# Kernel tuning notes

Measured on AMD Instinct MI355X. Metric: run time of the kernel, lower is better.

The kernel has to match this reference:

```python
import jax, jax.numpy as jnp
import numpy as np

TOP_K = 6  # num_experts_per_tok


def _glu_mlp(x, wg, wu, wd):
    # DeepSeek MLP: down( silu(gate(x)) * up(x) )
    return (jax.nn.silu(x @ wg) * (x @ wu)) @ wd


def setup_inputs() -> dict:
    key = jax.random.key(0)
    ks = jax.random.split(key, 8)
    B, S, D, E, F, FS = 2, 2048, 1024, 8, 512, 1024
    sc = 0.02
    return {
        "hidden_states": jax.random.normal(ks[0], (B, S, D), jnp.float32),
        "router_w": jax.random.normal(ks[1], (D, E), jnp.float32) * sc,
        "w_gate": jax.random.normal(ks[2], (E, D, F), jnp.float32) * sc,
        "w_up": jax.random.normal(ks[3], (E, D, F), jnp.float32) * sc,
        "w_down": jax.random.normal(ks[4], (E, F, D), jnp.float32) * sc,
        "ws_gate": jax.random.normal(ks[5], (D, FS), jnp.float32) * sc,
        "ws_up": jax.random.normal(ks[6], (D, FS), jnp.float32) * sc,
        "ws_down": jax.random.normal(ks[7], (FS, D), jnp.float32) * sc,
    }


def reference(hidden_states, router_w, w_gate, w_up, w_down, ws_gate, ws_up, ws_down):
    B, S, D = hidden_states.shape
    x = hidden_states.reshape(-1, D)                       # [T, D] tokens
    # Gate: softmax router + top-k (DeepSeek gate, no renorm)
    scores = jax.nn.softmax(x @ router_w, axis=-1)         # [T, E]
    topk_w, topk_idx = jax.lax.top_k(scores, TOP_K)        # [T, K]
    # Expert SiLU-GLU MLPs evaluated for all experts (math-identical to the
    # argsort dispatch -> grouped GEMM -> scatter combine in moe_infer)
    g = jnp.einsum('td,edf->etf', x, w_gate)               # [E, T, F]
    u = jnp.einsum('td,edf->etf', x, w_up)                 # [E, T, F]
    f_all = jnp.einsum('etf,efd->ted', jax.nn.silu(g) * u, w_down)  # [T, E, D]
    # Combine: final[t] = sum_k topk_w[t,k] * expert_{topk_idx[t,k]}(x[t])
    picked = jnp.take_along_axis(f_all, topk_idx[:, :, None], axis=1)  # [T, K, D]
    y = jnp.sum(picked * topk_w[:, :, None], axis=1).reshape(B, S, D)
    # shared experts branch
    y = y + _glu_mlp(hidden_states, ws_gate, ws_up, ws_down)
    return y
```

## Files before the change

### kernel.cpp

```cpp
#include <hip/hip_runtime.h>

typedef __attribute__((ext_vector_type(8))) short bf16x8;
typedef __attribute__((ext_vector_type(4))) float floatx4;

static __device__ __forceinline__ float b2f(unsigned short u) {
  union { unsigned int i; float f; } v; v.i = ((unsigned int)u) << 16; return v.f;
}
static __device__ __forceinline__ unsigned short f2b(float f) {
  union { float f; unsigned int i; } v; v.f = f;
  unsigned int x = v.i;
  return (unsigned short)((x + 0x7fffu + ((x >> 16) & 1u)) >> 16);
}

#define GLDS(gp, lp) \
  __builtin_amdgcn_global_load_lds( \
      (const __attribute__((address_space(1))) unsigned int*)(gp), \
      (__attribute__((address_space(3))) unsigned int*)(lp), 16, 0, 0)

static __device__ __forceinline__ void swizzle_mn(int lin, int Mb, int Nb,
                                                  int& m_idx, int& n_idx) {
  if ((Mb & 7) == 0) {
    int xcd = lin & 7;
    int idx = lin >> 3;
    int nstrips = Mb >> 3;
    m_idx = (idx % nstrips) * 8 + xcd;
    n_idx = idx / nstrips;
  } else {
    m_idx = lin % Mb;
    n_idx = lin / Mb;
  }
}

__global__ void cvt_f32_bf16(const float* __restrict__ src,
                             unsigned short* __restrict__ dst) {
  int i = (blockIdx.x * 256 + threadIdx.x) * 4;
  float4 v = *(const float4*)(src + i);
  ushort4 o;
  o.x = f2b(v.x); o.y = f2b(v.y); o.z = f2b(v.z); o.w = f2b(v.w);
  *(ushort4*)(dst + i) = o;
}

__global__ void transpose_f32_bf16_2(const float* __restrict__ sA,
                                     unsigned short* __restrict__ dA, int nzA,
                                     const float* __restrict__ sB,
                                     unsigned short* __restrict__ dB,
                                     int K, int N) {
  __shared__ unsigned short tile[32][33];
  int z = blockIdx.z;
  const float* src;
  unsigned short* dst;
  if (z < nzA) { src = sA + (size_t)z * K * N; dst = dA + (size_t)z * K * N; }
  else { src = sB + (size_t)(z - nzA) * K * N; dst = dB + (size_t)(z - nzA) * K * N; }
  const int bx = blockIdx.x * 32;
  const int by = blockIdx.y * 32;
  const int tx = threadIdx.x, ty = threadIdx.y;
#pragma unroll
  for (int i = 0; i < 4; i++)
    tile[ty + i * 8][tx] = f2b(src[(size_t)(by + ty + i * 8) * N + bx + tx]);
  __syncthreads();
#pragma unroll
  for (int i = 0; i < 4; i++)
    dst[(size_t)(bx + ty + i * 8) * K + by + tx] = tile[tx][ty + i * 8];
}

__global__ void transpose3_1024(const float* __restrict__ s0,
                                const float* __restrict__ s1,
                                const float* __restrict__ s2,
                                unsigned short* __restrict__ d0,
                                unsigned short* __restrict__ d1,
                                unsigned short* __restrict__ d2) {
  __shared__ unsigned short tile[32][33];
  const float* src = (blockIdx.z == 0) ? s0 : (blockIdx.z == 1) ? s1 : s2;
  unsigned short* dst = (blockIdx.z == 0) ? d0 : (blockIdx.z == 1) ? d1 : d2;
  const int bx = blockIdx.x * 32;
  const int by = blockIdx.y * 32;
  const int tx = threadIdx.x, ty = threadIdx.y;
#pragma unroll
  for (int i = 0; i < 4; i++)
    tile[ty + i * 8][tx] = f2b(src[(size_t)(by + ty + i * 8) * 1024 + bx + tx]);
  __syncthreads();
#pragma unroll
  for (int i = 0; i < 4; i++)
    dst[(size_t)(bx + ty + i * 8) * 1024 + by + tx] = tile[tx][ty + i * 8];
}

__global__ void router_topk(const float* __restrict__ X,
                            const float* __restrict__ RW,
                            float* __restrict__ cw) {
  const int t = blockIdx.x;
  const int lane = threadIdx.x;
  float acc[8];
#pragma unroll
  for (int e = 0; e < 8; e++) acc[e] = 0.f;
  for (int d = lane; d < 1024; d += 64) {
    float xv = X[(size_t)t * 1024 + d];
    const float* r = RW + d * 8;
    float4 r0 = *(const float4*)r;
    float4 r1 = *(const float4*)(r + 4);
    acc[0] += xv * r0.x; acc[1] += xv * r0.y;
    acc[2] += xv * r0.z; acc[3] += xv * r0.w;
    acc[4] += xv * r1.x; acc[5] += xv * r1.y;
    acc[6] += xv * r1.z; acc[7] += xv * r1.w;
  }
#pragma unroll
  for (int m = 1; m < 64; m <<= 1) {
#pragma unroll
    for (int e = 0; e < 8; e++) acc[e] += __shfl_xor(acc[e], m);
  }
  if (lane == 0) {
    float mx = acc[0];
#pragma unroll
    for (int e = 1; e < 8; e++) mx = fmaxf(mx, acc[e]);
    float prob[8], s = 0.f;
#pragma unroll
    for (int e = 0; e < 8; e++) { prob[e] = expf(acc[e] - mx); s += prob[e]; }
    float inv = 1.f / s;
#pragma unroll
    for (int e = 0; e < 8; e++) prob[e] *= inv;
    int m1 = 0;
#pragma unroll
    for (int e = 1; e < 8; e++) if (prob[e] < prob[m1]) m1 = e;
    int m2 = -1;
#pragma unroll
    for (int e = 0; e < 8; e++)
      if (e != m1 && (m2 < 0 || prob[e] < prob[m2])) m2 = e;
#pragma unroll
    for (int e = 0; e < 8; e++)
      cw[(size_t)t * 8 + e] = (e == m1 || e == m2) ? 0.f : prob[e];
  }
}

#define VMCNT(N) asm volatile("s_waitcnt vmcnt(" #N ")" ::: "memory")
#define BARS() do { __builtin_amdgcn_s_barrier(); \
                    __builtin_amdgcn_sched_barrier(0); } while (0)

#define STG_I0(K, BS) do { \
  GLDS(a0 + (K),          sm + (BS) + wid * 512); \
  GLDS(a0 + (K) + 131072, sm + (BS) + 8192 + wid * 512); } while (0)
#define STG_I1(K, BS) do { \
  GLDS(bg0 + (K),        sm + (BS) + 16384 + wid * 1024); \
  GLDS(bg0 + (K) + 8192, sm + (BS) + 16384 + wid * 1024 + 512); } while (0)
#define STG_I2(K, BS) do { \
  GLDS(bu0 + (K),        sm + (BS) + 24576 + wid * 1024); \
  GLDS(bu0 + (K) + 8192, sm + (BS) + 24576 + wid * 1024 + 512); } while (0)
#define STG_I3(K, BS) do { \
  GLDS(a0 + (K) + 65536,  sm + (BS) + 4096 + wid * 512); \
  GLDS(a0 + (K) + 196608, sm + (BS) + 12288 + wid * 512); } while (0)

#define READ_A(DST, DB, H) do { _Pragma("unroll") \
  for (int mf = 0; mf < 4; ++mf) { \
    const int row_ = wm * 128 + (H) * 64 + mf * 16 + lr; \
    const int rb_ = (DB) + row_ * 64; const int rx_ = row_ & 7; \
    DST[mf][0] = *(const bf16x8*)(sm + rb_ + ((quad ^ rx_) << 3)); \
    DST[mf][1] = *(const bf16x8*)(sm + rb_ + (((4 + quad) ^ rx_) << 3)); \
  } } while (0)

#define READ_B(DST, DB, RG) do { _Pragma("unroll") \
  for (int nf = 0; nf < 2; ++nf) { \
    const int row_ = wn * 32 + nf * 16 + lr; \
    const int rb_ = (DB) + (RG) + row_ * 64; const int rx_ = row_ & 7; \
    DST[nf][0] = *(const bf16x8*)(sm + rb_ + ((quad ^ rx_) << 3)); \
    DST[nf][1] = *(const bf16x8*)(sm + rb_ + (((4 + quad) ^ rx_) << 3)); \
  } } while (0)

#define MM(ACC, AF, BF) do { \
  __builtin_amdgcn_s_setprio(1); \
  _Pragma("unroll") \
  for (int mf = 0; mf < 4; ++mf) { _Pragma("unroll") \
    for (int nf = 0; nf < 2; ++nf) { \
      ACC[mf][nf] = __builtin_amdgcn_mfma_f32_16x16x32_bf16( \
          AF[mf][0], BF[nf][0], ACC[mf][nf], 0, 0, 0); \
      ACC[mf][nf] = __builtin_amdgcn_mfma_f32_16x16x32_bf16( \
          AF[mf][1], BF[nf][1], ACC[mf][nf], 0, 0, 0); \
    } } \
  __builtin_amdgcn_s_setprio(0); } while (0)

__global__ __launch_bounds__(512, 2) void gemm_gu_fused(
    const unsigned short* __restrict__ X,
    const unsigned short* __restrict__ WgTe,
    const unsigned short* __restrict__ WgTs,
    const unsigned short* __restrict__ WuTe,
    const unsigned short* __restrict__ WuTs,
    unsigned short* __restrict__ H,
    const float* __restrict__ cw, int Mb) {
  __shared__ __align__(16) unsigned short sm[65536];
  const int tid = threadIdx.x;
  const int wid = tid >> 6, lane = tid & 63;
  const int lr = lane & 15, quad = lane >> 4;
  const int wm = wid >> 2, wn = wid & 3;

  int m_idx, n_idx;
  {
    int lin = blockIdx.x;
    if ((Mb & 7) == 0) {
      int xcd = lin & 7, idx = lin >> 3;
      n_idx = idx % 40;
      m_idx = (idx / 40) * 8 + xcd;
    } else {
      m_idx = lin % Mb;
      n_idx = lin / Mb;
    }
  }
  const int m0 = m_idx * 256;
  const int n0 = n_idx * 128;

  const unsigned short *Bg, *Bu;
  int eidx = -1;
  if (n0 < 4096) {
    eidx = n0 >> 9;
    size_t off = ((size_t)eidx * 512 + (n0 & 511)) * 1024;
    Bg = WgTe + off; Bu = WuTe + off;
  } else {
    size_t off = (size_t)(n0 - 4096) * 1024;
    Bg = WgTs + off; Bu = WuTs + off;
  }

  const int grow8 = lane >> 3;
  const int gcol = ((lane & 7) ^ grow8) << 3;
  const unsigned short* a0 =
      X + (size_t)(m0 + wid * 8 + grow8) * 1024 + gcol;
  const unsigned short* bg0 =
      Bg + (size_t)(wid * 16 + grow8) * 1024 + gcol;
  const unsigned short* bu0 =
      Bu + (size_t)(wid * 16 + grow8) * 1024 + gcol;

  floatx4 gg[2][4][2], uu[2][4][2];
#pragma unroll
  for (int h = 0; h < 2; h++)
#pragma unroll
    for (int mf = 0; mf < 4; mf++)
#pragma unroll
      for (int nf = 0; nf < 2; nf++) {
        gg[h][mf][nf] = (floatx4)0.f;
        uu[h][mf][nf] = (floatx4)0.f;
      }

  bf16x8 fA0[4][2], fA1[4][2], fBg[2][2], fBu[2][2];

  STG_I0(0, 0); STG_I1(0, 0); STG_I2(0, 0); STG_I3(0, 0);

  for (int t = 0; t < 15; ++t) {
    const int db = (t & 1) << 15;
    const int nb = 32768 - db;
    const int kn = (t + 1) * 64;
    STG_I0(kn, nb);
    VMCNT(6); BARS();
    READ_A(fA0, db, 0);
    READ_B(fBg, db, 16384);
    MM(gg[0], fA0, fBg);
    STG_I1(kn, nb);
    VMCNT(6); BARS();
    READ_B(fBu, db, 24576);
    MM(uu[0], fA0, fBu);
    STG_I2(kn, nb);
    VMCNT(6); BARS();
    READ_A(fA1, db, 1);
    MM(gg[1], fA1, fBg);
    STG_I3(kn, nb);
    BARS();
    MM(uu[1], fA1, fBu);
  }
  {
    const int db = 32768;
    VMCNT(4); BARS();
    READ_A(fA0, db, 0);
    READ_B(fBg, db, 16384);
    MM(gg[0], fA0, fBg);
    VMCNT(2); BARS();
    READ_B(fBu, db, 24576);
    MM(uu[0], fA0, fBu);
    VMCNT(0); BARS();
    READ_A(fA1, db, 1);
    MM(gg[1], fA1, fBg);
    MM(uu[1], fA1, fBu);
  }

#pragma unroll
  for (int h = 0; h < 2; h++) {
#pragma unroll
    for (int mf = 0; mf < 4; mf++) {
#pragma unroll
      for (int nf = 0; nf < 2; nf++) {
#pragma unroll
        for (int r = 0; r < 4; r++) {
          int row = m0 + wm * 128 + h * 64 + mf * 16 + quad * 4 + r;
          int col = n0 + wn * 32 + nf * 16 + lr;
          float g = gg[h][mf][nf][r];
          float u = uu[h][mf][nf][r];
          float s = (eidx >= 0) ? cw[(size_t)row * 8 + eidx] : 1.0f;
          float silu = g / (1.0f + __expf(-g));
          H[(size_t)row * 5120 + col] = f2b(s * silu * u);
        }
      }
    }
  }
}

#define DN_STG(KN, SBUF) do { \
  GLDS(Ha + (size_t)(KN),          smD + (SBUF) + wid * 512); \
  GLDS(Ha + (size_t)(KN) + 327680, smD + (SBUF) + 4096 + wid * 512); \
  const unsigned short *b0p_, *b1p_; \
  if ((KN) < 4096) { \
    const unsigned short* be_ = WdTe + ((size_t)((KN) >> 9)) * (1024 * 512) + ((KN) & 511); \
    b0p_ = be_ + (size_t)bn0 * 512 + gcol; \
    b1p_ = be_ + (size_t)(bn0 + 64) * 512 + gcol; \
  } else { \
    b0p_ = WdTs + (size_t)bn0 * 1024 + ((KN) - 4096) + gcol; \
    b1p_ = WdTs + (size_t)(bn0 + 64) * 1024 + ((KN) - 4096) + gcol; \
  } \
  GLDS(b0p_, smD + (SBUF) + 8192 + wid * 512); \
  GLDS(b1p_, smD + (SBUF) + 12288 + wid * 512); } while (0)

#define DN_TILE(T, BUF, SBUF, DOSTG, VM) do { \
  VMCNT(VM); BARS(); \
  if (DOSTG) { DN_STG(((T) + 2) * 64, SBUF); } \
  bf16x8 af_[4][2], bf_[2][2]; \
  _Pragma("unroll") \
  for (int mt = 0; mt < 4; ++mt) { \
    const int row_ = wm * 64 + mt * 16 + lr; \
    const int rb_ = (BUF) + row_ * 64; const int rx_ = row_ & 7; \
    af_[mt][0] = *(const bf16x8*)(smD + rb_ + ((quad ^ rx_) << 3)); \
    af_[mt][1] = *(const bf16x8*)(smD + rb_ + (((4 + quad) ^ rx_) << 3)); \
  } \
  _Pragma("unroll") \
  for (int nt = 0; nt < 2; ++nt) { \
    const int row_ = wn * 32 + nt * 16 + lr; \
    const int rb_ = (BUF) + 8192 + row_ * 64; const int rx_ = row_ & 7; \
    bf_[nt][0] = *(const bf16x8*)(smD + rb_ + ((quad ^ rx_) << 3)); \
    bf_[nt][1] = *(const bf16x8*)(smD + rb_ + (((4 + quad) ^ rx_) << 3)); \
  } \
  __builtin_amdgcn_s_setprio(1); \
  _Pragma("unroll") \
  for (int kt = 0; kt < 2; ++kt) \
    _Pragma("unroll") \
    for (int mt = 0; mt < 4; ++mt) \
      _Pragma("unroll") \
      for (int nt = 0; nt < 2; ++nt) \
        acc[mt][nt] = __builtin_amdgcn_mfma_f32_16x16x32_bf16( \
            af_[mt][kt], bf_[nt][kt], acc[mt][nt], 0, 0, 0); \
  __builtin_amdgcn_s_setprio(0); } while (0)

__global__ __launch_bounds__(512, 2) void gemm_down(
    const unsigned short* __restrict__ H,
    const unsigned short* __restrict__ WdTe,
    const unsigned short* __restrict__ WdTs,
    float* __restrict__ Y, int Mb) {
  __shared__ __align__(16) unsigned short smD[49152];
  const int tid = threadIdx.x;
  const int wid = tid >> 6, lane = tid & 63;
  const int lr = lane & 15, quad = lane >> 4;
  const int wm = wid >> 2, wn = wid & 3;
  int m_idx, n_idx;
  swizzle_mn(blockIdx.x, Mb, 8, m_idx, n_idx);
  const int m0 = m_idx * 128;
  const int n0 = n_idx * 128;

  const int grow8 = lane >> 3;
  const int gcol = ((lane & 7) ^ grow8) << 3;
  const unsigned short* Ha = H + (size_t)(m0 + wid * 8 + grow8) * 5120 + gcol;
  const int bn0 = n0 + wid * 8 + grow8;

  floatx4 acc[4][2];
#pragma unroll
  for (int i = 0; i < 4; i++)
#pragma unroll
    for (int j = 0; j < 2; j++) acc[i][j] = (floatx4)0.f;

  DN_STG(0, 0);
  DN_STG(64, 16384);

  for (int t = 0; t < 78; t += 3) {
    DN_TILE(t,     0,     32768, true, 4);
    DN_TILE(t + 1, 16384, 0,     true, 4);
    DN_TILE(t + 2, 32768, 16384, true, 4);
  }
  DN_TILE(78, 0,     0, false, 4);
  DN_TILE(79, 16384, 0, false, 0);

#pragma unroll
  for (int mt = 0; mt < 4; mt++)
#pragma unroll
    for (int nt = 0; nt < 2; nt++)
#pragma unroll
      for (int r = 0; r < 4; r++) {
        int row = m0 + wm * 64 + mt * 16 + quad * 4 + r;
        int col = n0 + wn * 32 + nt * 16 + lr;
        Y[(size_t)row * 1024 + col] = acc[mt][nt][r];
      }
}

extern "C" void kernel_launch(void* const* d_in, const int* in_sizes, int n_in,
                              void* d_out, int out_size, void* d_ws, size_t ws_size,
                              hipStream_t stream) {
  const float* hs  = (const float*)d_in[0];
  const float* rw  = (const float*)d_in[1];
  const float* wg  = (const float*)d_in[2];
  const float* wu  = (const float*)d_in[3];
  const float* wd  = (const float*)d_in[4];
  const float* wsg = (const float*)d_in[5];
  const float* wsu = (const float*)d_in[6];
  const float* wsd = (const float*)d_in[7];
  float* out = (float*)d_out;

  char* p = (char*)d_ws;
  float* cw = (float*)p;                    p += (size_t)4096 * 8 * 4;
  unsigned short* Xb   = (unsigned short*)p; p += (size_t)4096 * 1024 * 2;
  unsigned short* wgT  = (unsigned short*)p; p += (size_t)8 * 512 * 1024 * 2;
  unsigned short* wuT  = (unsigned short*)p; p += (size_t)8 * 512 * 1024 * 2;
  unsigned short* wsgT = (unsigned short*)p; p += (size_t)1024 * 1024 * 2;
  unsigned short* wsuT = (unsigned short*)p; p += (size_t)1024 * 1024 * 2;
  unsigned short* wdT  = (unsigned short*)p; p += (size_t)8 * 1024 * 512 * 2;
  unsigned short* wsdT = (unsigned short*)p; p += (size_t)1024 * 1024 * 2;
  unsigned short* GH   = (unsigned short*)p;
  const size_t base_bytes = (size_t)(p - (char*)d_ws);

  int chunks = 8;
  for (int c = 1; c <= 8; c *= 2) {
    size_t gh_bytes = ((size_t)4096 / c) * 5120 * 2;
    if (base_bytes + gh_bytes <= ws_size) { chunks = c; break; }
  }
  const int rows = 4096 / chunks;
  const int Mb = rows / 128;
  const int MbG = rows / 256;

  dim3 tb(32, 8);
  cvt_f32_bf16<<<4096, 256, 0, stream>>>(hs, Xb);
  router_topk<<<4096, 64, 0, stream>>>(hs, rw, cw);
  transpose_f32_bf16_2<<<dim3(16, 32, 16), tb, 0, stream>>>(
      wg, wgT, 8, wu, wuT, 1024, 512);
  transpose_f32_bf16_2<<<dim3(32, 16, 8), tb, 0, stream>>>(
      wd, wdT, 8, wd, wdT, 512, 1024);
  transpose3_1024<<<dim3(32, 32, 3), tb, 0, stream>>>(
      wsg, wsu, wsd, wsgT, wsuT, wsdT);

  for (int c = 0; c < chunks; c++) {
    const unsigned short* Xc = Xb + (size_t)c * rows * 1024;
    const float* cwc = cw + (size_t)c * rows * 8;
    float* outc = out + (size_t)c * rows * 1024;
    gemm_gu_fused<<<MbG * 40, 512, 0, stream>>>(
        Xc, wgT, wsgT, wuT, wsuT, GH, cwc, MbG);
    gemm_down<<<Mb * 8, 512, 0, stream>>>(GH, wdT, wsdT, outc, Mb);
  }
}
```

Before: 292.8 us.

## Fuse router with input conversion, merge weight transposes, deepen down-GEMM pipeline

Merges the bf16 conversion of the hidden states into the router/top-k kernel so the activations are read once, with four tokens handled per block. Replaces the three weight-transpose launches with a single kernel that uses 64x64 tiles, vectorized float4 reads and 16-byte writes. Deepens the down-projection GEMM from a 3-stage to a 4-stage LDS pipeline, raising shared memory to 128KB per block. The goal is fewer launches, less memory traffic in preprocessing and better latency hiding, but the larger LDS footprint may reduce how many blocks fit on a CU alongside launch_bounds(512,2).

```diff
diff --git a/kernel.cpp b/kernel.cpp
--- a/kernel.cpp
+++ b/kernel.cpp
@@ -1,11 +1,9 @@
 #include <hip/hip_runtime.h>
 
 typedef __attribute__((ext_vector_type(8))) short bf16x8;
+typedef __attribute__((ext_vector_type(8))) unsigned short ushort8;
 typedef __attribute__((ext_vector_type(4))) float floatx4;
 
-static __device__ __forceinline__ float b2f(unsigned short u) {
-  union { unsigned int i; float f; } v; v.i = ((unsigned int)u) << 16; return v.f;
-}
 static __device__ __forceinline__ unsigned short f2b(float f) {
   union { float f; unsigned int i; } v; v.f = f;
   unsigned int x = v.i;
@@ -31,76 +29,35 @@
   }
 }
 
-__global__ void cvt_f32_bf16(const float* __restrict__ src,
-                             unsigned short* __restrict__ dst) {
-  int i = (blockIdx.x * 256 + threadIdx.x) * 4;
-  float4 v = *(const float4*)(src + i);
-  ushort4 o;
-  o.x = f2b(v.x); o.y = f2b(v.y); o.z = f2b(v.z); o.w = f2b(v.w);
-  *(ushort4*)(dst + i) = o;
-}
-
-__global__ void transpose_f32_bf16_2(const float* __restrict__ sA,
-                                     unsigned short* __restrict__ dA, int nzA,
-                                     const float* __restrict__ sB,
-                                     unsigned short* __restrict__ dB,
-                                     int K, int N) {
-  __shared__ unsigned short tile[32][33];
-  int z = blockIdx.z;
-  const float* src;
-  unsigned short* dst;
-  if (z < nzA) { src = sA + (size_t)z * K * N; dst = dA + (size_t)z * K * N; }
-  else { src = sB + (size_t)(z - nzA) * K * N; dst = dB + (size_t)(z - nzA) * K * N; }
-  const int bx = blockIdx.x * 32;
-  const int by = blockIdx.y * 32;
-  const int tx = threadIdx.x, ty = threadIdx.y;
-#pragma unroll
-  for (int i = 0; i < 4; i++)
-    tile[ty + i * 8][tx] = f2b(src[(size_t)(by + ty + i * 8) * N + bx + tx]);
-  __syncthreads();
-#pragma unroll
-  for (int i = 0; i < 4; i++)
-    dst[(size_t)(bx + ty + i * 8) * K + by + tx] = tile[tx][ty + i * 8];
-}
-
-__global__ void transpose3_1024(const float* __restrict__ s0,
-                                const float* __restrict__ s1,
-                                const float* __restrict__ s2,
-                                unsigned short* __restrict__ d0,
-                                unsigned short* __restrict__ d1,
-                                unsigned short* __restrict__ d2) {
-  __shared__ unsigned short tile[32][33];
-  const float* src = (blockIdx.z == 0) ? s0 : (blockIdx.z == 1) ? s1 : s2;
-  unsigned short* dst = (blockIdx.z == 0) ? d0 : (blockIdx.z == 1) ? d1 : d2;
-  const int bx = blockIdx.x * 32;
-  const int by = blockIdx.y * 32;
-  const int tx = threadIdx.x, ty = threadIdx.y;
-#pragma unroll
-  for (int i = 0; i < 4; i++)
-    tile[ty + i * 8][tx] = f2b(src[(size_t)(by + ty + i * 8) * 1024 + bx + tx]);
-  __syncthreads();
-#pragma unroll
-  for (int i = 0; i < 4; i++)
-    dst[(size_t)(bx + ty + i * 8) * 1024 + by + tx] = tile[tx][ty + i * 8];
-}
-
-__global__ void router_topk(const float* __restrict__ X,
-                            const float* __restrict__ RW,
-                            float* __restrict__ cw) {
-  const int t = blockIdx.x;
-  const int lane = threadIdx.x;
+__global__ __launch_bounds__(256) void router_cvt(
+    const float* __restrict__ X, const float* __restrict__ RW,
+    float* __restrict__ cw, unsigned short* __restrict__ Xb) {
+  const int tid = threadIdx.x;
+  const int wid = tid >> 6, lane = tid & 63;
+  const int t = blockIdx.x * 4 + wid;
+  const float* xp = X + (size_t)t * 1024;
+  unsigned short* xo = Xb + (size_t)t * 1024;
   float acc[8];
 #pragma unroll
   for (int e = 0; e < 8; e++) acc[e] = 0.f;
-  for (int d = lane; d < 1024; d += 64) {
-    float xv = X[(size_t)t * 1024 + d];
-    const float* r = RW + d * 8;
-    float4 r0 = *(const float4*)r;
-    float4 r1 = *(const float4*)(r + 4);
-    acc[0] += xv * r0.x; acc[1] += xv * r0.y;
-    acc[2] += xv * r0.z; acc[3] += xv * r0.w;
-    acc[4] += xv * r1.x; acc[5] += xv * r1.y;
-    acc[6] += xv * r1.z; acc[7] += xv * r1.w;
+#pragma unroll
+  for (int i = 0; i < 4; i++) {
+    const int d0 = i * 256 + lane * 4;
+    float4 v = *(const float4*)(xp + d0);
+    ushort4 o;
+    o.x = f2b(v.x); o.y = f2b(v.y); o.z = f2b(v.z); o.w = f2b(v.w);
+    *(ushort4*)(xo + d0) = o;
+    const float xv[4] = {v.x, v.y, v.z, v.w};
+#pragma unroll
+    for (int j = 0; j < 4; j++) {
+      const float* r = RW + (size_t)(d0 + j) * 8;
+      float4 r0 = *(const float4*)r;
+      float4 r1 = *(const float4*)(r + 4);
+      acc[0] += xv[j] * r0.x; acc[1] += xv[j] * r0.y;
+      acc[2] += xv[j] * r0.z; acc[3] += xv[j] * r0.w;
+      acc[4] += xv[j] * r1.x; acc[5] += xv[j] * r1.y;
+      acc[6] += xv[j] * r1.z; acc[7] += xv[j] * r1.w;
+    }
   }
 #pragma unroll
   for (int m = 1; m < 64; m <<= 1) {
@@ -127,6 +84,52 @@
 #pragma unroll
     for (int e = 0; e < 8; e++)
       cw[(size_t)t * 8 + e] = (e == m1 || e == m2) ? 0.f : prob[e];
+  }
+}
+
+__global__ __launch_bounds__(256) void transpose_all(
+    const float* __restrict__ wg, const float* __restrict__ wu,
+    const float* __restrict__ wd, const float* __restrict__ wsg,
+    const float* __restrict__ wsu, const float* __restrict__ wsd,
+    unsigned short* __restrict__ wgT, unsigned short* __restrict__ wuT,
+    unsigned short* __restrict__ wdT, unsigned short* __restrict__ wsgT,
+    unsigned short* __restrict__ wsuT, unsigned short* __restrict__ wsdT) {
+  __shared__ __align__(16) unsigned short T[64 * 68];
+  const int z = blockIdx.z;
+  const float* src; unsigned short* dst; int K, N;
+  if (z < 8)       { src = wg  + (size_t)z * 1024 * 512;        dst = wgT + (size_t)z * 512 * 1024;        K = 1024; N = 512; }
+  else if (z < 16) { src = wu  + (size_t)(z - 8) * 1024 * 512;  dst = wuT + (size_t)(z - 8) * 512 * 1024;  K = 1024; N = 512; }
+  else if (z < 24) { src = wd  + (size_t)(z - 16) * 512 * 1024; dst = wdT + (size_t)(z - 16) * 1024 * 512; K = 512;  N = 1024; }
+  else if (z == 24){ src = wsg; dst = wsgT; K = 1024; N = 1024; }
+  else if (z == 25){ src = wsu; dst = wsuT; K = 1024; N = 1024; }
+  else             { src = wsd; dst = wsdT; K = 1024; N = 1024; }
+  const int bn = blockIdx.x * 64, bk = blockIdx.y * 64;
+  if (bn >= N || bk >= K) return;
+  const int tid = threadIdx.x;
+  {
+    const int r = tid >> 4;
+    const int c = (tid & 15) * 4;
+#pragma unroll
+    for (int i = 0; i < 4; i++) {
+      const int rr = r + i * 16;
+      float4 v = *(const float4*)(src + (size_t)(bk + rr) * N + bn + c);
+      ushort4 o;
+      o.x = f2b(v.x); o.y = f2b(v.y); o.z = f2b(v.z); o.w = f2b(v.w);
+      *(ushort4*)(&T[rr * 68 + c]) = o;
+    }
+  }
+  __syncthreads();
+  {
+    const int n_ = tid >> 3;
+    const int k0 = (tid & 7) * 8;
+#pragma unroll
+    for (int p = 0; p < 2; p++) {
+      const int n = n_ + p * 32;
+      ushort8 o;
+#pragma unroll
+      for (int j = 0; j < 8; j++) o[j] = T[(k0 + j) * 68 + n];
+      *(ushort8*)(dst + (size_t)(bn + n) * K + bk + k0) = o;
+    }
   }
 }
 
@@ -313,7 +316,7 @@
 
 #define DN_TILE(T, BUF, SBUF, DOSTG, VM) do { \
   VMCNT(VM); BARS(); \
-  if (DOSTG) { DN_STG(((T) + 2) * 64, SBUF); } \
+  if (DOSTG) { DN_STG(((T) + 3) * 64, SBUF); } \
   bf16x8 af_[4][2], bf_[2][2]; \
   _Pragma("unroll") \
   for (int mt = 0; mt < 4; ++mt) { \
@@ -345,7 +348,7 @@
     const unsigned short* __restrict__ WdTe,
     const unsigned short* __restrict__ WdTs,
     float* __restrict__ Y, int Mb) {
-  __shared__ __align__(16) unsigned short smD[49152];
+  __shared__ __align__(16) unsigned short smD[65536];
   const int tid = threadIdx.x;
   const int wid = tid >> 6, lane = tid & 63;
   const int lr = lane & 15, quad = lane >> 4;
@@ -368,14 +371,18 @@
 
   DN_STG(0, 0);
   DN_STG(64, 16384);
-
-  for (int t = 0; t < 78; t += 3) {
-    DN_TILE(t,     0,     32768, true, 4);
-    DN_TILE(t + 1, 16384, 0,     true, 4);
-    DN_TILE(t + 2, 32768, 16384, true, 4);
-  }
-  DN_TILE(78, 0,     0, false, 4);
-  DN_TILE(79, 16384, 0, false, 0);
+  DN_STG(128, 32768);
+
+  for (int t = 0; t < 76; t += 4) {
+    DN_TILE(t,     0,     49152, true, 8);
+    DN_TILE(t + 1, 16384, 0,     true, 8);
+    DN_TILE(t + 2, 32768, 16384, true, 8);
+    DN_TILE(t + 3, 49152, 32768, true, 8);
+  }
+  DN_TILE(76, 0,     49152, true,  8);
+  DN_TILE(77, 16384, 0,     false, 8);
+  DN_TILE(78, 32768, 0,     false, 4);
+  DN_TILE(79, 49152, 0,     false, 0);
 
 #pragma unroll
   for (int mt = 0; mt < 4; mt++)
@@ -423,15 +430,9 @@
   const int Mb = rows / 128;
   const int MbG = rows / 256;
 
-  dim3 tb(32, 8);
-  cvt_f32_bf16<<<4096, 256, 0, stream>>>(hs, Xb);
-  router_topk<<<4096, 64, 0, stream>>>(hs, rw, cw);
-  transpose_f32_bf16_2<<<dim3(16, 32, 16), tb, 0, stream>>>(
-      wg, wgT, 8, wu, wuT, 1024, 512);
-  transpose_f32_bf16_2<<<dim3(32, 16, 8), tb, 0, stream>>>(
-      wd, wdT, 8, wd, wdT, 512, 1024);
-  transpose3_1024<<<dim3(32, 32, 3), tb, 0, stream>>>(
-      wsg, wsu, wsd, wsgT, wsuT, wsdT);
+  router_cvt<<<1024, 256, 0, stream>>>(hs, rw, cw, Xb);
+  transpose_all<<<dim3(16, 16, 27), 256, 0, stream>>>(
+      wg, wu, wd, wsg, wsu, wsd, wgT, wuT, wdT, wsgT, wsuT, wsdT);
 
   for (int c = 0; c < chunks; c++) {
     const unsigned short* Xc = Xb + (size_t)c * rows * 1024;
```

Result: faster. 287.0 us (-2.0%).
